# Kernel optimization log

Hardware: AMD Instinct MI355X
Metric: run time of the kernel (lower is better)

## Reference

```python
import jax, jax.numpy as jnp
import numpy as np
import math

H = 1024
B, S = 4, 2048

def setup_inputs() -> dict:
    key = jax.random.key(0)
    k0, k1, k2, k3, k4 = jax.random.split(key, 5)
    scale = 1.0 / math.sqrt(H)
    return {
        "input_seq_rep": jax.random.normal(k0, (B, S, H), dtype=jnp.float32),
        "Wk": jax.random.uniform(k1, (H, H), dtype=jnp.float32, minval=-scale, maxval=scale),
        "bk": jax.random.uniform(k2, (H,), dtype=jnp.float32, minval=-scale, maxval=scale),
        "Wq": jax.random.uniform(k3, (H, H), dtype=jnp.float32, minval=-scale, maxval=scale),
        "bq": jax.random.uniform(k4, (H,), dtype=jnp.float32, minval=-scale, maxval=scale),
        "k_mul": 64,
    }

def reference(input_seq_rep, Wk, bk, Wq, bq, k_mul):
    b, s, h = input_seq_rep.shape
    x = jax.nn.relu(input_seq_rep)
    # torch Linear: x @ W.T + b
    k = jnp.einsum('bsh,oh->bso', x, Wk) + bk   # key (also used as value)
    q = jnp.einsum('bsh,oh->bso', x, Wq) + bq
    scores = jnp.einsum('bqh,bkh->bqk', q, k) / jnp.sqrt(jnp.float32(h))
    # Faithful mask: banded window only for batch index 0; other batches all-zero mask
    i = jnp.arange(s)[:, None]
    j = jnp.arange(s)[None, :]
    band = ((j <= i) & (j >= i - k_mul)).astype(jnp.float32)  # (S,S)
    mask = jnp.zeros((b, s, s), dtype=jnp.float32).at[0].set(band)
    scores = jnp.where(mask == 0, jnp.float32(-1e9), scores)
    p_attn = jax.nn.softmax(scores, axis=-1)
    out = jnp.einsum('bqk,bkh->bqh', p_attn, k)
    return out, p_attn
```

## Files before the change

kernel.cpp:

```cpp
#include <hip/hip_runtime.h>

#define SD 2048
#define HD 1024
#define BD 4

typedef __bf16 bf16_t;
typedef bf16_t bf16x8 __attribute__((ext_vector_type(8)));
typedef float f32x4 __attribute__((ext_vector_type(4)));
typedef unsigned short ushortx8 __attribute__((ext_vector_type(8)));
typedef unsigned short ushort_t;

__device__ inline unsigned short f2bf(float f) {
  return __builtin_bit_cast(unsigned short, (__bf16)f);
}

__device__ inline void gload_lds16(const void* g, void* l) {
  __builtin_amdgcn_global_load_lds(
      (const __attribute__((address_space(1))) void*)g,
      (__attribute__((address_space(3))) void*)l, 16, 0, 0);
}

template <int ROWS>
__device__ inline void stage_rows(const ushort_t* __restrict__ src, int r0, int k0,
                                  int tid, ushort_t* lds)
{
#pragma unroll
  for (int it = 0; it < ROWS / 32; ++it) {
    int c   = it * 256 + tid;
    int row = c >> 3;
    int kc8 = c & 7;
    int kcs = kc8 ^ (row & 7);
    gload_lds16(&src[(size_t)(r0 + row) * HD + k0 + kcs * 8], &lds[c * 8]);
  }
}

__device__ inline bf16x8 lds_frag(const ushort_t* l, int row, int kc8) {
  int kcs = kc8 ^ (row & 7);
  return *(const bf16x8*)&l[row * 64 + kcs * 8];
}

__global__ __launch_bounds__(256) void prep(
    const float* __restrict__ X, const float* __restrict__ Wk,
    const float* __restrict__ Wq, ushort_t* __restrict__ Xb,
    ushort_t* __restrict__ Wkb, ushort_t* __restrict__ Wqb,
    float* __restrict__ part, float* __restrict__ patRest)
{
  const int bid = blockIdx.x;
  const int t = threadIdx.x;
  if (bid < 96) {
    const int b = bid >> 5;
    const int sub = bid & 31;
    const float4* Xp = (const float4*)(X + (size_t)(b + 1) * SD * HD + (size_t)sub * 64 * HD);
    float4 acc = make_float4(0.f, 0.f, 0.f, 0.f);
#pragma unroll 4
    for (int rr = 0; rr < 64; ++rr) {
      float4 v = Xp[rr * 256 + t];
      acc.x += fmaxf(v.x, 0.f); acc.y += fmaxf(v.y, 0.f);
      acc.z += fmaxf(v.z, 0.f); acc.w += fmaxf(v.w, 0.f);
    }
    ((float4*)part)[((size_t)b * 32 + sub) * 256 + t] = acc;
    return;
  }
  const int n8x = SD * HD / 8;
  const int n8w = HD * HD / 8;
  const int ncvt = n8x + 2 * n8w;
  const int nfill = 3 * SD * (SD / 4);
  const int total = ncvt + nfill;
  const int stride = 2336 * 256;
  const float uf = 1.0f / SD;
  for (int e = (bid - 96) * 256 + t; e < total; e += stride) {
    if (e >= ncvt) {
      ((float4*)patRest)[e - ncvt] = make_float4(uf, uf, uf, uf);
      continue;
    }
    const float4* s4; ushortx8* d8; int idx; bool relu;
    if (e < n8x)            { s4 = (const float4*)X;  d8 = (ushortx8*)Xb;  idx = e;             relu = true; }
    else if (e < n8x + n8w) { s4 = (const float4*)Wk; d8 = (ushortx8*)Wkb; idx = e - n8x;       relu = false; }
    else                    { s4 = (const float4*)Wq; d8 = (ushortx8*)Wqb; idx = e - n8x - n8w; relu = false; }
    float4 a = s4[idx * 2], b4 = s4[idx * 2 + 1];
    float v[8] = {a.x, a.y, a.z, a.w, b4.x, b4.y, b4.z, b4.w};
    ushortx8 o;
#pragma unroll
    for (int j = 0; j < 8; ++j) {
      float f = v[j];
      if (relu) f = fmaxf(f, 0.0f);
      o[j] = f2bf(f);
    }
    d8[idx] = o;
  }
}

__global__ __launch_bounds__(256, 2) void gemm_kq(
    const ushort_t* __restrict__ Xb, const ushort_t* __restrict__ Wkb,
    const ushort_t* __restrict__ Wqb, const float* __restrict__ bk,
    const float* __restrict__ bq, float* __restrict__ Kf,
    ushort_t* __restrict__ Kb, ushort_t* __restrict__ Qb)
{
  const int bm = blockIdx.x, bn = blockIdx.y;
  const int half = bn >> 4;
  const ushort_t* Bm = half ? Wqb : Wkb;
  const int m0 = bm * 128, n0 = (bn & 15) * 64;

  const int tid = threadIdx.x;
  const int lane = tid & 63;
  const int wave = tid >> 6;
  const int wm = wave >> 1, wn = wave & 1;

  __shared__ __align__(16) ushort_t lA[2][8192];
  __shared__ __align__(16) ushort_t lB[2][4096];

  f32x4 acc[4][2] = {};

  stage_rows<128>(Xb, m0, 0, tid, lA[0]);
  stage_rows<64>(Bm, n0, 0, tid, lB[0]);
  __syncthreads();

  for (int t = 0; t < 16; ++t) {
    const int cur = t & 1;
    if (t < 15) {
      stage_rows<128>(Xb, m0, (t + 1) * 64, tid, lA[cur ^ 1]);
      stage_rows<64>(Bm, n0, (t + 1) * 64, tid, lB[cur ^ 1]);
    }
#pragma unroll
    for (int h = 0; h < 2; ++h) {
      bf16x8 af[4], bfr[2];
#pragma unroll
      for (int mi = 0; mi < 4; ++mi)
        af[mi] = lds_frag(lA[cur], wm * 64 + mi * 16 + (lane & 15), h * 4 + (lane >> 4));
#pragma unroll
      for (int ni = 0; ni < 2; ++ni)
        bfr[ni] = lds_frag(lB[cur], wn * 32 + ni * 16 + (lane & 15), h * 4 + (lane >> 4));
#pragma unroll
      for (int mi = 0; mi < 4; ++mi)
#pragma unroll
        for (int ni = 0; ni < 2; ++ni)
          acc[mi][ni] = __builtin_amdgcn_mfma_f32_16x16x32_bf16(af[mi], bfr[ni], acc[mi][ni], 0, 0, 0);
    }
    __syncthreads();
  }

  const int rb = (lane >> 4) * 4;
  const int cc = lane & 15;
  const float* bias = half ? bq : bk;
#pragma unroll
  for (int ni = 0; ni < 2; ++ni) {
    int col = n0 + wn * 32 + ni * 16 + cc;
    float bv = bias[col];
#pragma unroll
    for (int mi = 0; mi < 4; ++mi) {
#pragma unroll
      for (int j = 0; j < 4; ++j) {
        int row = m0 + wm * 64 + mi * 16 + rb + j;
        float v = acc[mi][ni][j] + bv;
        size_t off = (size_t)row * HD + col;
        if (!half) { Kf[off] = v; Kb[off] = f2bf(v); }
        else       { Qb[off] = f2bf(v); }
      }
    }
  }
}

__global__ __launch_bounds__(256, 2) void band_cm(
    const ushort_t* __restrict__ Q, const ushort_t* __restrict__ K,
    float* __restrict__ Sb0, float* __restrict__ Sb1,
    const float* __restrict__ part, const float* __restrict__ Wk,
    const float* __restrict__ bk, float* __restrict__ cm)
{
  __shared__ __align__(16) char smem[32768];
  const int bid = blockIdx.x;
  const int tid = threadIdx.x;

  if (bid < 126) {
    const int tt = bid >> 1;
    const int ks = bid & 1;
    const int blk = (tt + 1) >> 1;
    const int tcol = (tt + 1) & 1;
    const int m0 = blk * 64;
    const int n0 = (blk - 1 + tcol) * 64;
    float* Sb = ks ? Sb1 : Sb0;

    const int lane = tid & 63;
    const int wave = tid >> 6;
    const int wm = wave >> 1, wn = wave & 1;

    ushort_t* lA = (ushort_t*)smem;
    ushort_t* lB = (ushort_t*)(smem + 16384);

    f32x4 acc[2][2] = {};

    const int kbase = ks * 512;
    stage_rows<64>(Q, m0, kbase, tid, lA);
    stage_rows<64>(K, n0, kbase, tid, lB);
    __syncthreads();

    for (int t = 0; t < 8; ++t) {
      const int cur = t & 1;
      if (t < 7) {
        stage_rows<64>(Q, m0, kbase + (t + 1) * 64, tid, lA + (cur ^ 1) * 4096);
        stage_rows<64>(K, n0, kbase + (t + 1) * 64, tid, lB + (cur ^ 1) * 4096);
      }
#pragma unroll
      for (int h = 0; h < 2; ++h) {
        bf16x8 af[2], bfr[2];
#pragma unroll
        for (int mi = 0; mi < 2; ++mi)
          af[mi] = lds_frag(lA + cur * 4096, wm * 32 + mi * 16 + (lane & 15), h * 4 + (lane >> 4));
#pragma unroll
        for (int ni = 0; ni < 2; ++ni)
          bfr[ni] = lds_frag(lB + cur * 4096, wn * 32 + ni * 16 + (lane & 15), h * 4 + (lane >> 4));
#pragma unroll
        for (int mi = 0; mi < 2; ++mi)
#pragma unroll
          for (int ni = 0; ni < 2; ++ni)
            acc[mi][ni] = __builtin_amdgcn_mfma_f32_16x16x32_bf16(af[mi], bfr[ni], acc[mi][ni], 0, 0, 0);
      }
      __syncthreads();
    }

    const int rb = (lane >> 4) * 4;
    const int cc = lane & 15;
#pragma unroll
    for (int ni = 0; ni < 2; ++ni) {
      int ccol = tcol * 64 + wn * 32 + ni * 16 + cc;
#pragma unroll
      for (int mi = 0; mi < 2; ++mi)
#pragma unroll
        for (int j = 0; j < 4; ++j) {
          int row = m0 + wm * 32 + mi * 16 + rb + j;
          Sb[(size_t)row * 128 + ccol] = acc[mi][ni][j] * 0.03125f;
        }
    }
    return;
  }

  {
    const int cid = bid - 126;
    const int b = cid >> 4, og = cid & 15;
    float* xs = (float*)smem;
#pragma unroll
    for (int k = 0; k < 4; ++k) {
      int h = tid + 256 * k;
      float a = 0;
#pragma unroll 8
      for (int rc = 0; rc < 32; ++rc) a += part[((size_t)b * 32 + rc) * HD + h];
      xs[h] = a;
    }
    __syncthreads();
    const int o = og * 64 + (tid >> 2);
    const int q = tid & 3;
    const f32x4* wr = (const f32x4*)(Wk + (size_t)o * HD);
    const f32x4* x4 = (const f32x4*)xs;
    float a = 0;
#pragma unroll 8
    for (int i = 0; i < 64; ++i) {
      f32x4 w = wr[q * 64 + i], x = x4[q * 64 + i];
      a += w[0] * x[0] + w[1] * x[1] + w[2] * x[2] + w[3] * x[3];
    }
    a += __shfl_xor(a, 1);
    a += __shfl_xor(a, 2);
    if (q == 0) cm[b * HD + o] = a * (1.0f / SD) + bk[o];
  }
}

__global__ __launch_bounds__(256, 2) void pv_epi(
    const float* __restrict__ Sb0, const float* __restrict__ Sb1,
    const float* __restrict__ Kf, const float* __restrict__ cm,
    float* __restrict__ out0, float* __restrict__ P0,
    float* __restrict__ out123)
{
  __shared__ __align__(16) float smem[15488];
  const int bid = blockIdx.x;
  const int t = threadIdx.x;

  if (bid < 512) {
    float* Ks  = smem;
    float* spl = smem + 12288;
    const int i0 = (bid >> 3) * 32;
    const int hc = bid & 7;

    const f32x4* K4 = (const f32x4*)Kf;
    for (int e = t; e < 96 * 32; e += 256) {
      int lr = e >> 5, c4 = e & 31;
      int gr = i0 - 64 + lr;
      if (gr < 0) gr = 0;
      *(f32x4*)&Ks[lr * 128 + c4 * 4] = K4[(size_t)gr * 256 + hc * 32 + c4];
    }

    {
      const int r = t >> 3, sub = t & 7;
      const int i = i0 + r;
      const int jlo = (i >= 64) ? i - 64 : 0;
      const int scoff = i0 & 32;
      float sv[12];
      float m = -1e30f;
#pragma unroll
      for (int k = 0; k < 12; ++k) {
        int lj = sub + 8 * k;
        int gj = i0 - 64 + lj;
        bool val = (gj >= jlo) && (gj <= i);
        float s = -1e30f;
        if (val) {
          size_t sidx = (size_t)i * 128 + lj + scoff;
          s = Sb0[sidx] + Sb1[sidx];
        }
        sv[k] = s;
        m = fmaxf(m, s);
      }
#pragma unroll
      for (int off = 1; off < 8; off <<= 1) m = fmaxf(m, __shfl_xor(m, off));
      float p[12], sum = 0;
#pragma unroll
      for (int k = 0; k < 12; ++k) {
        p[k] = (sv[k] > -1e29f) ? __expf(sv[k] - m) : 0.0f;
        sum += p[k];
      }
#pragma unroll
      for (int off = 1; off < 8; off <<= 1) sum += __shfl_xor(sum, off);
      float inv = 1.0f / sum;
#pragma unroll
      for (int k = 0; k < 12; ++k) spl[r * 100 + sub + 8 * k] = p[k] * inv;
    }
    __syncthreads();

    const int r = t >> 3;
    const int g = t & 7;
    f32x4 a0 = {0,0,0,0}, a1 = {0,0,0,0}, a2 = {0,0,0,0}, a3 = {0,0,0,0};
    for (int lj = 0; lj < 96; ++lj) {
      float pv = spl[r * 100 + lj];
      const float* kr = &Ks[lj * 128 + g * 4];
      a0 += pv * *(const f32x4*)(kr);
      a1 += pv * *(const f32x4*)(kr + 32);
      a2 += pv * *(const f32x4*)(kr + 64);
      a3 += pv * *(const f32x4*)(kr + 96);
    }
    float* ob = out0 + (size_t)(i0 + r) * HD + hc * 128 + g * 4;
    *(f32x4*)(ob)      = a0;
    *(f32x4*)(ob + 32) = a1;
    *(f32x4*)(ob + 64) = a2;
    *(f32x4*)(ob + 96) = a3;
    return;
  }

  if (bid < 1024) {
    float* probs = smem;
    const int widx = t >> 6;
    const int lane = t & 63;
    const int i = (bid - 512) * 4 + widx;
    const int jlo = (i >= 64) ? i - 64 : 0;
    const int cnt = i - jlo + 1;
    const int base = ((i >> 6) - 1) * 64;

    float s0 = -1e30f;
    if (lane < cnt) {
      size_t c = (size_t)i * 128 + (jlo - base + lane);
      s0 = Sb0[c] + Sb1[c];
    }
    float s1 = -1e30f;
    if (cnt == 65) {
      size_t c = (size_t)i * 128 + (jlo - base + 64);
      s1 = Sb0[c] + Sb1[c];
    }
    float m = s0;
#pragma unroll
    for (int off = 1; off < 64; off <<= 1) m = fmaxf(m, __shfl_xor(m, off));
    m = fmaxf(m, s1);
    float p0 = (lane < cnt) ? __expf(s0 - m) : 0.0f;
    float p1 = (cnt == 65) ? __expf(s1 - m) : 0.0f;
    float sum = p0;
#pragma unroll
    for (int off = 1; off < 64; off <<= 1) sum += __shfl_xor(sum, off);
    sum += p1;
    float inv = 1.0f / sum;
    if (lane < cnt) probs[widx * 68 + lane] = p0 * inv;
    if (lane == 0 && cnt == 65) probs[widx * 68 + 64] = p1 * inv;
    __syncthreads();

    float4* rowp = (float4*)(P0 + (size_t)i * SD);
#pragma unroll
    for (int k = 0; k < 8; ++k) {
      int f4i = k * 64 + lane;
      int j0 = f4i * 4;
      float4 v = make_float4(0.f, 0.f, 0.f, 0.f);
      if (j0 + 3 >= jlo && j0 <= i) {
        float* vv = (float*)&v;
#pragma unroll
        for (int q = 0; q < 4; ++q) {
          int j = j0 + q;
          if (j >= jlo && j <= i) vv[q] = probs[widx * 68 + (j - jlo)];
        }
      }
      rowp[f4i] = v;
    }
    return;
  }

  {
    const int nf4 = 3 * SD * (HD / 4);
    const int per_b = SD * (HD / 4);
    const f32x4* cm4 = (const f32x4*)cm;
    f32x4* o4 = (f32x4*)out123;
    for (int idx = (bid - 1024) * 256 + t; idx < nf4; idx += 512 * 256) {
      int b = idx / per_b;
      int h4 = idx & (HD / 4 - 1);
      o4[idx] = cm4[b * (HD / 4) + h4];
    }
  }
}

extern "C" void kernel_launch(void* const* d_in, const int* in_sizes, int n_in,
                              void* d_out, int out_size, void* d_ws, size_t ws_size,
                              hipStream_t stream)
{
  (void)in_sizes; (void)n_in; (void)out_size; (void)ws_size;
  const float* X  = (const float*)d_in[0];
  const float* Wk = (const float*)d_in[1];
  const float* bk = (const float*)d_in[2];
  const float* Wq = (const float*)d_in[3];
  const float* bq = (const float*)d_in[4];

  float* out = (float*)d_out;
  float* pat = out + (size_t)BD * SD * HD;

  char* w = (char*)d_ws;
  ushort_t* Xb   = (ushort_t*)w; w += (size_t)SD * HD * 2;
  ushort_t* Wkb  = (ushort_t*)w; w += (size_t)HD * HD * 2;
  ushort_t* Wqb  = (ushort_t*)w; w += (size_t)HD * HD * 2;
  float*    Kf0  = (float*)w;    w += (size_t)SD * HD * 4;
  ushort_t* Kb0  = (ushort_t*)w; w += (size_t)SD * HD * 2;
  ushort_t* Q0b  = (ushort_t*)w; w += (size_t)SD * HD * 2;
  float*    part = (float*)w;    w += (size_t)3 * 32 * HD * 4;
  float*    cm   = (float*)w;    w += (size_t)3 * HD * 4;
  float*    Sb0  = (float*)w;    w += (size_t)SD * 128 * 4;
  float*    Sb1  = (float*)w;    w += (size_t)SD * 128 * 4;

  prep<<<2432, 256, 0, stream>>>(X, Wk, Wq, Xb, Wkb, Wqb, part, pat + (size_t)SD * SD);
  gemm_kq<<<dim3(16, 32), 256, 0, stream>>>(Xb, Wkb, Wqb, bk, bq, Kf0, Kb0, Q0b);
  band_cm<<<174, 256, 0, stream>>>(Q0b, Kb0, Sb0, Sb1, part, Wk, bk, cm);
  pv_epi<<<1536, 256, 0, stream>>>(Sb0, Sb1, Kf0, cm, out, pat, out + (size_t)SD * HD);
}
```

Measured before the change: 76.53 us.

## Overlap uniform p_attn fill with K/Q GEMM and drop fp32 K copy

The constant 1/S fill of p_attn for batches 1-3 (about 50 MB) moves out of the prep kernel and into extra blocks interleaved with the GEMM tiles, 3 fill blocks per 4 GEMM blocks. The bandwidth-bound fill can then run alongside the compute-bound MFMA GEMM. The fp32 copy of K is also removed: the GEMM writes only bf16 K, and pv_epi converts bf16 to fp32 when staging K into LDS. This cuts global writes and reads but feeds bf16-rounded K into the P·V product, which costs some accuracy.

```diff
diff --git a/kernel.cpp b/kernel.cpp
--- a/kernel.cpp
+++ b/kernel.cpp
@@ -12,6 +12,10 @@
 
 __device__ inline unsigned short f2bf(float f) {
   return __builtin_bit_cast(unsigned short, (__bf16)f);
+}
+
+__device__ inline float bf2f(unsigned short u) {
+  return __builtin_bit_cast(float, (unsigned)u << 16);
 }
 
 __device__ inline void gload_lds16(const void* g, void* l) {
@@ -43,7 +47,7 @@
     const float* __restrict__ X, const float* __restrict__ Wk,
     const float* __restrict__ Wq, ushort_t* __restrict__ Xb,
     ushort_t* __restrict__ Wkb, ushort_t* __restrict__ Wqb,
-    float* __restrict__ part, float* __restrict__ patRest)
+    float* __restrict__ part)
 {
   const int bid = blockIdx.x;
   const int t = threadIdx.x;
@@ -63,16 +67,9 @@
   }
   const int n8x = SD * HD / 8;
   const int n8w = HD * HD / 8;
-  const int ncvt = n8x + 2 * n8w;
-  const int nfill = 3 * SD * (SD / 4);
-  const int total = ncvt + nfill;
-  const int stride = 2336 * 256;
-  const float uf = 1.0f / SD;
+  const int total = n8x + 2 * n8w;
+  const int stride = 2048 * 256;
   for (int e = (bid - 96) * 256 + t; e < total; e += stride) {
-    if (e >= ncvt) {
-      ((float4*)patRest)[e - ncvt] = make_float4(uf, uf, uf, uf);
-      continue;
-    }
     const float4* s4; ushortx8* d8; int idx; bool relu;
     if (e < n8x)            { s4 = (const float4*)X;  d8 = (ushortx8*)Xb;  idx = e;             relu = true; }
     else if (e < n8x + n8w) { s4 = (const float4*)Wk; d8 = (ushortx8*)Wkb; idx = e - n8x;       relu = false; }
@@ -93,21 +90,35 @@
 __global__ __launch_bounds__(256, 2) void gemm_kq(
     const ushort_t* __restrict__ Xb, const ushort_t* __restrict__ Wkb,
     const ushort_t* __restrict__ Wqb, const float* __restrict__ bk,
-    const float* __restrict__ bq, float* __restrict__ Kf,
-    ushort_t* __restrict__ Kb, ushort_t* __restrict__ Qb)
-{
-  const int bm = blockIdx.x, bn = blockIdx.y;
+    const float* __restrict__ bq, ushort_t* __restrict__ Kb,
+    ushort_t* __restrict__ Qb, float* __restrict__ patRest)
+{
+  __shared__ __align__(16) ushort_t lA[2][8192];
+  __shared__ __align__(16) ushort_t lB[2][4096];
+
+  const int bid = blockIdx.x;
+  const int g7 = bid / 7, r7 = bid % 7;
+  const int tid = threadIdx.x;
+
+  if (r7 >= 4) {
+    const int f = g7 * 3 + (r7 - 4);
+    const int nf4 = 3 * SD * (SD / 4);
+    const float uf = 1.0f / SD;
+    float4 v = make_float4(uf, uf, uf, uf);
+    float4* p4 = (float4*)patRest;
+    for (int e = f * 256 + tid; e < nf4; e += 384 * 256) p4[e] = v;
+    return;
+  }
+
+  const int idx = g7 * 4 + r7;
+  const int bm = idx >> 5, bn = idx & 31;
   const int half = bn >> 4;
   const ushort_t* Bm = half ? Wqb : Wkb;
   const int m0 = bm * 128, n0 = (bn & 15) * 64;
 
-  const int tid = threadIdx.x;
   const int lane = tid & 63;
   const int wave = tid >> 6;
   const int wm = wave >> 1, wn = wave & 1;
-
-  __shared__ __align__(16) ushort_t lA[2][8192];
-  __shared__ __align__(16) ushort_t lB[2][4096];
 
   f32x4 acc[4][2] = {};
 
@@ -142,6 +153,7 @@
   const int rb = (lane >> 4) * 4;
   const int cc = lane & 15;
   const float* bias = half ? bq : bk;
+  ushort_t* dst = half ? Qb : Kb;
 #pragma unroll
   for (int ni = 0; ni < 2; ++ni) {
     int col = n0 + wn * 32 + ni * 16 + cc;
@@ -151,10 +163,7 @@
 #pragma unroll
       for (int j = 0; j < 4; ++j) {
         int row = m0 + wm * 64 + mi * 16 + rb + j;
-        float v = acc[mi][ni][j] + bv;
-        size_t off = (size_t)row * HD + col;
-        if (!half) { Kf[off] = v; Kb[off] = f2bf(v); }
-        else       { Qb[off] = f2bf(v); }
+        dst[(size_t)row * HD + col] = f2bf(acc[mi][ni][j] + bv);
       }
     }
   }
@@ -264,7 +273,7 @@
 
 __global__ __launch_bounds__(256, 2) void pv_epi(
     const float* __restrict__ Sb0, const float* __restrict__ Sb1,
-    const float* __restrict__ Kf, const float* __restrict__ cm,
+    const ushort_t* __restrict__ Kb, const float* __restrict__ cm,
     float* __restrict__ out0, float* __restrict__ P0,
     float* __restrict__ out123)
 {
@@ -278,12 +287,15 @@
     const int i0 = (bid >> 3) * 32;
     const int hc = bid & 7;
 
-    const f32x4* K4 = (const f32x4*)Kf;
-    for (int e = t; e < 96 * 32; e += 256) {
-      int lr = e >> 5, c4 = e & 31;
+    for (int e = t; e < 96 * 16; e += 256) {
+      int lr = e >> 4, c8 = e & 15;
       int gr = i0 - 64 + lr;
       if (gr < 0) gr = 0;
-      *(f32x4*)&Ks[lr * 128 + c4 * 4] = K4[(size_t)gr * 256 + hc * 32 + c4];
+      ushortx8 u = *(const ushortx8*)&Kb[(size_t)gr * HD + hc * 128 + c8 * 8];
+      f32x4 f0 = {bf2f(u[0]), bf2f(u[1]), bf2f(u[2]), bf2f(u[3])};
+      f32x4 f1 = {bf2f(u[4]), bf2f(u[5]), bf2f(u[6]), bf2f(u[7])};
+      *(f32x4*)&Ks[lr * 128 + c8 * 8]     = f0;
+      *(f32x4*)&Ks[lr * 128 + c8 * 8 + 4] = f1;
     }
 
     {
@@ -425,7 +437,6 @@
   ushort_t* Xb   = (ushort_t*)w; w += (size_t)SD * HD * 2;
   ushort_t* Wkb  = (ushort_t*)w; w += (size_t)HD * HD * 2;
   ushort_t* Wqb  = (ushort_t*)w; w += (size_t)HD * HD * 2;
-  float*    Kf0  = (float*)w;    w += (size_t)SD * HD * 4;
   ushort_t* Kb0  = (ushort_t*)w; w += (size_t)SD * HD * 2;
   ushort_t* Q0b  = (ushort_t*)w; w += (size_t)SD * HD * 2;
   float*    part = (float*)w;    w += (size_t)3 * 32 * HD * 4;
@@ -433,8 +444,8 @@
   float*    Sb0  = (float*)w;    w += (size_t)SD * 128 * 4;
   float*    Sb1  = (float*)w;    w += (size_t)SD * 128 * 4;
 
-  prep<<<2432, 256, 0, stream>>>(X, Wk, Wq, Xb, Wkb, Wqb, part, pat + (size_t)SD * SD);
-  gemm_kq<<<dim3(16, 32), 256, 0, stream>>>(Xb, Wkb, Wqb, bk, bq, Kf0, Kb0, Q0b);
+  prep<<<2144, 256, 0, stream>>>(X, Wk, Wq, Xb, Wkb, Wqb, part);
+  gemm_kq<<<896, 256, 0, stream>>>(Xb, Wkb, Wqb, bk, bq, Kb0, Q0b, pat + (size_t)SD * SD);
   band_cm<<<174, 256, 0, stream>>>(Q0b, Kb0, Sb0, Sb1, part, Wk, bk, cm);
-  pv_epi<<<1536, 256, 0, stream>>>(Sb0, Sb1, Kf0, cm, out, pat, out + (size_t)SD * HD);
-}
+  pv_epi<<<1536, 256, 0, stream>>>(Sb0, Sb1, Kb0, cm, out, pat, out + (size_t)SD * HD);
+}
```

New measurement: 73.93 us. 3.4% less time.
